# Kernel tuning notes

Measured on AMD Instinct MI355X. Metric: run time of the kernel, lower is better.

## Reference

```python
import jax, jax.numpy as jnp
import numpy as np

B, C, N, M = 4, 256, 4096, 4096
H, D = 4, 64  # num_heads, head_dim = C // H


def _proj(x, W, b):
    # Conv1d(kernel_size=1): pointwise linear over channel dim. x:(B,Cin,L) W:(Cout,Cin) b:(Cout,)
    return jnp.einsum('oc,bcn->bon', W, x) + b[None, :, None]


def setup_inputs() -> dict:
    key = jax.random.key(0)
    ks = jax.random.split(key, 10)
    s = 1.0 / np.sqrt(C)
    return {
        'query': jax.random.normal(ks[0], (B, C, N), dtype=jnp.float32),
        'source': jax.random.normal(ks[1], (B, C, M), dtype=jnp.float32),
        'Wq': jax.random.normal(ks[2], (C, C), dtype=jnp.float32) * s,
        'bq': jnp.zeros((C,), dtype=jnp.float32),
        'Wk': jax.random.normal(ks[3], (C, C), dtype=jnp.float32) * s,
        'bk': jnp.zeros((C,), dtype=jnp.float32),
        'Wv': jax.random.normal(ks[4], (C, C), dtype=jnp.float32) * s,
        'bv': jnp.zeros((C,), dtype=jnp.float32),
        'Wm': jax.random.normal(ks[5], (C, C), dtype=jnp.float32) * s,
        'bm': jnp.zeros((C,), dtype=jnp.float32),
    }


def reference(query, source, Wq, bq, Wk, bk, Wv, bv, Wm, bm):
    b = query.shape[0]
    n = query.shape[-1]
    Q = _proj(query, Wq, bq).reshape(b, H, D, -1)   # (B,H,D,N)
    K = _proj(source, Wk, bk).reshape(b, H, D, -1)  # (B,H,D,M)
    V = _proj(source, Wv, bv).reshape(b, H, D, -1)  # (B,H,D,M)
    scores = jnp.einsum('bhdn,bhdm->bhnm', Q, K) / (D ** 0.5)
    attn = jax.nn.softmax(scores, axis=-1)
    out = jnp.einsum('bhnm,bhdm->bhdn', attn, V)    # (B,H,D,N)
    out = out.reshape(b, H * D, n)                   # (B,C,N)
    return _proj(out, Wm, bm)
```

## Files before the change

### kernel.cpp

```cpp
#include <hip/hip_runtime.h>
#include <hip/hip_bf16.h>
#include <stdint.h>

#define BB 4
#define CCH 256
#define NN 4096
#define MM 4096
#define HH 4
#define DDIM 64

typedef __attribute__((ext_vector_type(8))) short short8v;
typedef __attribute__((ext_vector_type(4))) float f32x4;
typedef __attribute__((ext_vector_type(16))) float f32x16;

__device__ __forceinline__ unsigned short f2b(float f) {
    unsigned int u = __builtin_bit_cast(unsigned int, f);
    unsigned int r = (u + 0x7FFFu + ((u >> 16) & 1u)) >> 16;
    return (unsigned short)r;
}

__device__ __forceinline__ f32x16 zero16() {
    f32x16 z;
#pragma unroll
    for (int i = 0; i < 16; i++) z[i] = 0.f;
    return z;
}

__global__ __launch_bounds__(256) void convert_kernel(
    const float* __restrict__ q, const float* __restrict__ s,
    const float* __restrict__ Wq, const float* __restrict__ Wk,
    const float* __restrict__ Wv, const float* __restrict__ Wm,
    unsigned short* __restrict__ XTq, unsigned short* __restrict__ XTs,
    unsigned short* __restrict__ Wb) {
    __shared__ float tile[64][65];
    const int bid = blockIdx.x, tid = threadIdx.x;
    if (bid < 2048) {
        const float* in = (bid < 1024) ? q : s;
        unsigned short* out = (bid < 1024) ? XTq : XTs;
        const int r = bid & 1023;
        const int b = r >> 8;
        const int rr = r & 255;
        const int l0 = (rr >> 2) * 64, c0 = (rr & 3) * 64;
#pragma unroll
        for (int i = 0; i < 16; i++) {
            int idx = tid + (i << 8);
            int cc = idx >> 6, ll = idx & 63;
            tile[cc][ll] = in[(size_t)(b * CCH + c0 + cc) * 4096 + l0 + ll];
        }
        __syncthreads();
#pragma unroll
        for (int i = 0; i < 16; i++) {
            int idx = tid + (i << 8);
            int ll = idx >> 6, cc = idx & 63;
            out[((size_t)(b * 4096 + l0 + ll) << 8) + c0 + cc] = f2b(tile[cc][ll]);
        }
    } else {
        const int wid = bid - 2048;
        const int wsel = wid >> 4;
        const float* src = (wsel == 0) ? Wq : (wsel == 1) ? Wk : (wsel == 2) ? Wv : Wm;
        const int off = (wid & 15) * 4096;
#pragma unroll
        for (int i = 0; i < 16; i++) {
            int idx = off + tid + (i << 8);
            Wb[(size_t)wsel * 65536 + idx] = f2b(src[idx]);
        }
    }
}

template <int OUTMODE, bool AHEAD>
__device__ __forceinline__ void gemm_body(const unsigned short* __restrict__ XT,
                                          const unsigned short* __restrict__ W,
                                          const float* __restrict__ bias,
                                          void* __restrict__ outv) {
    constexpr int WSTR = 264;
    constexpr int XSTR = 40;
    __shared__ __align__(16) unsigned short Wlds[64 * WSTR];
    __shared__ __align__(16) unsigned short Xlds[256 * XSTR];
    const int tid = threadIdx.x, w = tid >> 6, l = tid & 63;
    const int lg = l >> 4, lm = l & 15;
    const int n0 = blockIdx.x * 256, o0 = blockIdx.y * 64;
    const int oh = (w >> 1) * 32, nh = (w & 1) * 128;

#pragma unroll
    for (int i = 0; i < 8; i++) {
        int idx = tid + (i << 8);
        int row = idx >> 5, c8 = (idx & 31) * 8;
        *(uint4*)&Wlds[row * WSTR + c8] = *(const uint4*)&W[(size_t)(o0 + row) * 256 + c8];
    }

    f32x4 acc[8][2];
#pragma unroll
    for (int nt = 0; nt < 8; nt++)
#pragma unroll
        for (int ot = 0; ot < 2; ot++) acc[nt][ot] = (f32x4){0.f, 0.f, 0.f, 0.f};

    for (int kc = 0; kc < 8; kc++) {
#pragma unroll
        for (int i = 0; i < 4; i++) {
            int idx = tid + (i << 8);
            int row = idx >> 2;
            const unsigned short* srcp;
            if constexpr (AHEAD) {
                int c = kc * 32 + (idx & 3) * 8;
                srcp = XT + ((size_t)(c >> 6) * 4096 + n0 + row) * 64 + (c & 63);
            } else {
                srcp = XT + (size_t)(n0 + row) * 256 + kc * 32 + (idx & 3) * 8;
            }
            *(uint4*)&Xlds[row * XSTR + (idx & 3) * 8] = *(const uint4*)srcp;
        }
        __syncthreads();
        short8v bfrag[2];
#pragma unroll
        for (int ot = 0; ot < 2; ot++)
            bfrag[ot] = *(const short8v*)&Wlds[(oh + ot * 16 + lm) * WSTR + kc * 32 + lg * 8];
#pragma unroll
        for (int nt = 0; nt < 8; nt++) {
            short8v af = *(const short8v*)&Xlds[(nh + nt * 16 + lm) * XSTR + lg * 8];
            acc[nt][0] = __builtin_amdgcn_mfma_f32_16x16x32_bf16(af, bfrag[0], acc[nt][0], 0, 0, 0);
            acc[nt][1] = __builtin_amdgcn_mfma_f32_16x16x32_bf16(af, bfrag[1], acc[nt][1], 0, 0, 0);
        }
        __syncthreads();
    }

#pragma unroll
    for (int nt = 0; nt < 8; nt++)
#pragma unroll
        for (int ot = 0; ot < 2; ot++) {
            int o = o0 + oh + ot * 16 + lm;
            int nb = n0 + nh + nt * 16 + lg * 4;
            float bb = bias[o];
            if constexpr (OUTMODE == 2) {
                float* out = (float*)outv;
                float4 v = make_float4(acc[nt][ot][0] + bb, acc[nt][ot][1] + bb,
                                       acc[nt][ot][2] + bb, acc[nt][ot][3] + bb);
                *(float4*)&out[(size_t)o * 4096 + nb] = v;
            } else if constexpr (OUTMODE == 0) {
                unsigned short* out = (unsigned short*)outv;
                __align__(8) unsigned short v[4];
#pragma unroll
                for (int t = 0; t < 4; t++) v[t] = f2b(acc[nt][ot][t] + bb);
                *(uint2*)&out[(size_t)o * 4096 + nb] = *(uint2*)v;
            } else {
                unsigned short* out = (unsigned short*)outv;
                unsigned short* outp = out + ((size_t)(o >> 6) * 4096 + nb) * 64 + (o & 63);
#pragma unroll
                for (int t = 0; t < 4; t++) outp[t * 64] = f2b(acc[nt][ot][t] + bb);
            }
        }
}

__global__ __launch_bounds__(256) void gemm_qkv_kernel(
    const unsigned short* __restrict__ XTq, const unsigned short* __restrict__ XTs,
    const unsigned short* __restrict__ Wb,
    const float* __restrict__ bq, const float* __restrict__ bk, const float* __restrict__ bv,
    unsigned short* __restrict__ QT, unsigned short* __restrict__ KT,
    unsigned short* __restrict__ Vn) {
    const int z = blockIdx.z;
    const int b = z / 3, p = z - b * 3;
    const unsigned short* XT = ((p == 0) ? XTq : XTs) + (size_t)b * 4096 * 256;
    const unsigned short* W = Wb + p * 65536;
    const float* bias = (p == 0) ? bq : (p == 1) ? bk : bv;
    if (p == 2) {
        gemm_body<0, false>(XT, W, bias, Vn + (size_t)b * 256 * 4096);
    } else {
        unsigned short* out = ((p == 0) ? QT : KT) + (size_t)b * 1048576;
        gemm_body<1, false>(XT, W, bias, out);
    }
}

__global__ __launch_bounds__(256) void gemm_final_kernel(
    const unsigned short* __restrict__ OH, const unsigned short* __restrict__ Wm,
    const float* __restrict__ bm, float* __restrict__ out) {
    const int b = blockIdx.z;
    gemm_body<2, true>(OH + (size_t)b * 1048576, Wm, bm, out + (size_t)b * 256 * 4096);
}

__device__ __forceinline__ void stage_kv(const unsigned short* __restrict__ Kb,
                                         const unsigned short* __restrict__ Vb,
                                         char* dst, int m0s, int tid) {
    char* dK = dst;
    char* dV = dst + 8192;
#pragma unroll
    for (int i = 0; i < 2; i++) {
        int ch = tid + (i << 8);
        int rr = ch >> 3, pp = ch & 7;
        int sw = (pp ^ (rr & 7)) << 4;
        const char* sK = (const char*)(Kb + ((size_t)(m0s + rr) << 6)) + sw;
        const char* sV = (const char*)(Vb + (size_t)rr * 4096 + m0s) + sw;
        __builtin_amdgcn_global_load_lds(
            (const __attribute__((address_space(1))) unsigned int*)sK,
            (__attribute__((address_space(3))) unsigned int*)(dK + (ch << 4)), 16, 0, 0);
        __builtin_amdgcn_global_load_lds(
            (const __attribute__((address_space(1))) unsigned int*)sV,
            (__attribute__((address_space(3))) unsigned int*)(dV + (ch << 4)), 16, 0, 0);
    }
}

__global__ __launch_bounds__(256, 1) void attn_kernel(
    const unsigned short* __restrict__ QT, const unsigned short* __restrict__ KT,
    const unsigned short* __restrict__ Vn, unsigned short* __restrict__ OH) {
    __shared__ __align__(16) char smem[32768];
    const int tid = threadIdx.x, w = tid >> 6, l = tid & 63;
    const int lo5 = l & 31, hi = l >> 5;
    const int bh = blockIdx.y, b = bh >> 2, h = bh & 3;
    const int q0 = blockIdx.x * 256 + w * 64;
    const float s2 = 0.125f * 1.44269504f;

    short8v qf[2][4];
#pragma unroll
    for (int nc = 0; nc < 2; nc++) {
        size_t qrow = ((size_t)bh * 4096 + q0 + nc * 32 + lo5) * 64;
#pragma unroll
        for (int c = 0; c < 4; c++)
            qf[nc][c] = *(const short8v*)&QT[qrow + c * 16 + hi * 8];
    }

    const unsigned short* Vb = Vn + ((size_t)b * 256 + h * 64) * 4096;
    const unsigned short* Kb = KT + (size_t)bh * 262144;

    f32x16 o[2][2];
#pragma unroll
    for (int dc = 0; dc < 2; dc++)
#pragma unroll
        for (int nc = 0; nc < 2; nc++) o[dc][nc] = zero16();
    float mrun[2] = {-1e30f, -1e30f}, lrun[2] = {0.f, 0.f};

    stage_kv(Kb, Vb, smem, 0, tid);

    for (int it = 0; it < 64; it++) {
        __syncthreads();
        char* cur = smem + ((it & 1) << 14);
        if (it < 63) stage_kv(Kb, Vb, smem + (((it + 1) & 1) << 14), (it + 1) * 64, tid);

        short8v kf[2][4];
#pragma unroll
        for (int mc = 0; mc < 2; mc++) {
            int m = mc * 32 + lo5;
#pragma unroll
            for (int c = 0; c < 4; c++)
                kf[mc][c] = *(const short8v*)(cur + m * 128 + (((c * 2 + hi) * 16) ^ ((m & 7) << 4)));
        }
        short8v vf[2][4];
#pragma unroll
        for (int dc = 0; dc < 2; dc++) {
            int d = dc * 32 + lo5;
#pragma unroll
            for (int c = 0; c < 4; c++)
                vf[dc][c] = *(const short8v*)(cur + 8192 + d * 128 + (((c * 2 + hi) * 16) ^ ((d & 7) << 4)));
        }

        f32x16 s[2][2];
#pragma unroll
        for (int nc = 0; nc < 2; nc++)
#pragma unroll
            for (int mc = 0; mc < 2; mc++) {
                f32x16 a = zero16();
#pragma unroll
                for (int c = 0; c < 4; c++)
                    a = __builtin_amdgcn_mfma_f32_32x32x16_bf16(kf[mc][c], qf[nc][c], a, 0, 0, 0);
                s[nc][mc] = a;
            }

        float mxs[2];
#pragma unroll
        for (int nc = 0; nc < 2; nc++) {
            float tv[16];
#pragma unroll
            for (int r = 0; r < 16; r++) tv[r] = fmaxf(s[nc][0][r], s[nc][1][r]);
#pragma unroll
            for (int st = 8; st > 0; st >>= 1)
#pragma unroll
                for (int r = 0; r < st; r++) tv[r] = fmaxf(tv[r], tv[r + st]);
            float mx = fmaxf(tv[0], __shfl_xor(tv[0], 32));
            mxs[nc] = mx * s2;
        }
        if (__any((mxs[0] > mrun[0] + 8.f) || (mxs[1] > mrun[1] + 8.f))) {
#pragma unroll
            for (int nc = 0; nc < 2; nc++) {
                float mn = fmaxf(mrun[nc], mxs[nc]);
                float al = exp2f(mrun[nc] - mn);
                mrun[nc] = mn;
                lrun[nc] *= al;
#pragma unroll
                for (int dc = 0; dc < 2; dc++) o[dc][nc] = o[dc][nc] * al;
            }
        }

#pragma unroll
        for (int nc = 0; nc < 2; nc++) {
            float ls0 = 0.f, ls1 = 0.f, ls2 = 0.f, ls3 = 0.f;
            unsigned int pw[2][8];
#pragma unroll
            for (int mc = 0; mc < 2; mc++) {
                float p[16];
#pragma unroll
                for (int r = 0; r < 16; r++)
                    p[r] = exp2f(fmaf(s[nc][mc][r], s2, -mrun[nc]));
#pragma unroll
                for (int r = 0; r < 4; r++) {
                    ls0 += p[r];
                    ls1 += p[r + 4];
                    ls2 += p[r + 8];
                    ls3 += p[r + 12];
                }
#pragma unroll
                for (int half = 0; half < 2; half++)
#pragma unroll
                    for (int wdx = 0; wdx < 2; wdx++) {
                        unsigned int a, bq;
                        asm("v_cvt_pk_bf16_f32 %0, %1, %2"
                            : "=v"(a) : "v"(p[half * 8 + 2 * wdx]), "v"(p[half * 8 + 2 * wdx + 1]));
                        asm("v_cvt_pk_bf16_f32 %0, %1, %2"
                            : "=v"(bq) : "v"(p[half * 8 + 4 + 2 * wdx]), "v"(p[half * 8 + 4 + 2 * wdx + 1]));
                        asm volatile("v_permlane32_swap_b32 %0, %1" : "+v"(a), "+v"(bq));
                        pw[mc][half * 4 + wdx] = a;
                        pw[mc][half * 4 + wdx + 2] = bq;
                    }
            }
            lrun[nc] += (ls0 + ls1) + (ls2 + ls3);
#pragma unroll
            for (int dc = 0; dc < 2; dc++)
#pragma unroll
                for (int mc = 0; mc < 2; mc++)
#pragma unroll
                    for (int half = 0; half < 2; half++) {
                        union { unsigned int u[4]; short8v v; } pu;
#pragma unroll
                        for (int t = 0; t < 4; t++) pu.u[t] = pw[mc][half * 4 + t];
                        o[dc][nc] = __builtin_amdgcn_mfma_f32_32x32x16_bf16(
                            vf[dc][2 * mc + half], pu.v, o[dc][nc], 0, 0, 0);
                    }
        }
    }

    float inv[2];
#pragma unroll
    for (int nc = 0; nc < 2; nc++) {
        float lt = lrun[nc] + __shfl_xor(lrun[nc], 32);
        inv[nc] = 1.f / lt;
    }
    __syncthreads();
#pragma unroll
    for (int nc = 0; nc < 2; nc++) {
        int row = w * 64 + nc * 32 + lo5;
        char* rbase = smem + row * 128;
        int sw = (row & 7) << 4;
#pragma unroll
        for (int dc = 0; dc < 2; dc++)
#pragma unroll
            for (int g = 0; g < 4; g++) {
                ushort4 v4;
                v4.x = f2b(o[dc][nc][g * 4 + 0] * inv[nc]);
                v4.y = f2b(o[dc][nc][g * 4 + 1] * inv[nc]);
                v4.z = f2b(o[dc][nc][g * 4 + 2] * inv[nc]);
                v4.w = f2b(o[dc][nc][g * 4 + 3] * inv[nc]);
                int colb = dc * 64 + g * 16 + hi * 8;
                *(ushort4*)(rbase + (colb ^ sw)) = v4;
            }
    }
    __syncthreads();
    {
        int row = tid;
        size_t gbase = ((size_t)bh * 4096 + blockIdx.x * 256 + row) * 64;
        int sw = (row & 7) << 4;
#pragma unroll
        for (int ch = 0; ch < 8; ch++) {
            uint4 v = *(const uint4*)(smem + row * 128 + ((ch * 16) ^ sw));
            *(uint4*)&OH[gbase + ch * 8] = v;
        }
    }
}

extern "C" void kernel_launch(void* const* d_in, const int* in_sizes, int n_in,
                              void* d_out, int out_size, void* d_ws, size_t ws_size,
                              hipStream_t stream) {
    const float* q  = (const float*)d_in[0];
    const float* s  = (const float*)d_in[1];
    const float* Wq = (const float*)d_in[2];
    const float* bq = (const float*)d_in[3];
    const float* Wk = (const float*)d_in[4];
    const float* bk = (const float*)d_in[5];
    const float* Wv = (const float*)d_in[6];
    const float* bv = (const float*)d_in[7];
    const float* Wm = (const float*)d_in[8];
    const float* bm = (const float*)d_in[9];
    float* out = (float*)d_out;
    char* ws = (char*)d_ws;

    const size_t SZ = (size_t)BB * 4096 * 256 * 2;
    unsigned short* XTq  = (unsigned short*)(ws);
    unsigned short* XTs  = (unsigned short*)(ws + SZ);
    unsigned short* Wb   = (unsigned short*)(ws + 2 * SZ);
    unsigned short* QT   = (unsigned short*)(ws + 2 * SZ + 524288);
    unsigned short* KTh  = (unsigned short*)(ws + 3 * SZ + 524288);
    unsigned short* Vnat = (unsigned short*)(ws + 4 * SZ + 524288);
    unsigned short* OH   = XTq;

    convert_kernel<<<2112, 256, 0, stream>>>(q, s, Wq, Wk, Wv, Wm, XTq, XTs, Wb);
    gemm_qkv_kernel<<<dim3(16, 4, 12), 256, 0, stream>>>(XTq, XTs, Wb, bq, bk, bv,
                                                         QT, KTh, Vnat);
    attn_kernel<<<dim3(16, 16), 256, 0, stream>>>(QT, KTh, Vnat, OH);
    gemm_final_kernel<<<dim3(16, 4, 4), 256, 0, stream>>>(OH, Wb + 3 * 65536, bm, out);
}
```

Baseline: 273.7 us.

## Use 512-thread attention blocks with one query tile per wave; fold softmax scale into Q

```diff
diff --git a/kernel.cpp b/kernel.cpp
--- a/kernel.cpp
+++ b/kernel.cpp
@@ -71,7 +71,7 @@
 __device__ __forceinline__ void gemm_body(const unsigned short* __restrict__ XT,
                                           const unsigned short* __restrict__ W,
                                           const float* __restrict__ bias,
-                                          void* __restrict__ outv) {
+                                          void* __restrict__ outv, float oscale) {
     constexpr int WSTR = 264;
     constexpr int XSTR = 40;
     __shared__ __align__(16) unsigned short Wlds[64 * WSTR];
@@ -144,7 +144,7 @@
                 unsigned short* out = (unsigned short*)outv;
                 unsigned short* outp = out + ((size_t)(o >> 6) * 4096 + nb) * 64 + (o & 63);
 #pragma unroll
-                for (int t = 0; t < 4; t++) outp[t * 64] = f2b(acc[nt][ot][t] + bb);
+                for (int t = 0; t < 4; t++) outp[t * 64] = f2b((acc[nt][ot][t] + bb) * oscale);
             }
         }
 }
@@ -161,10 +161,10 @@
     const unsigned short* W = Wb + p * 65536;
     const float* bias = (p == 0) ? bq : (p == 1) ? bk : bv;
     if (p == 2) {
-        gemm_body<0, false>(XT, W, bias, Vn + (size_t)b * 256 * 4096);
+        gemm_body<0, false>(XT, W, bias, Vn + (size_t)b * 256 * 4096, 1.0f);
     } else {
         unsigned short* out = ((p == 0) ? QT : KT) + (size_t)b * 1048576;
-        gemm_body<1, false>(XT, W, bias, out);
+        gemm_body<1, false>(XT, W, bias, out, (p == 0) ? 0.1803368801f : 1.0f);
     }
 }
 
@@ -172,58 +172,48 @@
     const unsigned short* __restrict__ OH, const unsigned short* __restrict__ Wm,
     const float* __restrict__ bm, float* __restrict__ out) {
     const int b = blockIdx.z;
-    gemm_body<2, true>(OH + (size_t)b * 1048576, Wm, bm, out + (size_t)b * 256 * 4096);
+    gemm_body<2, true>(OH + (size_t)b * 1048576, Wm, bm, out + (size_t)b * 256 * 4096, 1.0f);
 }
 
 __device__ __forceinline__ void stage_kv(const unsigned short* __restrict__ Kb,
                                          const unsigned short* __restrict__ Vb,
                                          char* dst, int m0s, int tid) {
-    char* dK = dst;
-    char* dV = dst + 8192;
-#pragma unroll
-    for (int i = 0; i < 2; i++) {
-        int ch = tid + (i << 8);
-        int rr = ch >> 3, pp = ch & 7;
-        int sw = (pp ^ (rr & 7)) << 4;
-        const char* sK = (const char*)(Kb + ((size_t)(m0s + rr) << 6)) + sw;
-        const char* sV = (const char*)(Vb + (size_t)rr * 4096 + m0s) + sw;
-        __builtin_amdgcn_global_load_lds(
-            (const __attribute__((address_space(1))) unsigned int*)sK,
-            (__attribute__((address_space(3))) unsigned int*)(dK + (ch << 4)), 16, 0, 0);
-        __builtin_amdgcn_global_load_lds(
-            (const __attribute__((address_space(1))) unsigned int*)sV,
-            (__attribute__((address_space(3))) unsigned int*)(dV + (ch << 4)), 16, 0, 0);
-    }
-}
-
-__global__ __launch_bounds__(256, 1) void attn_kernel(
+    const int rr = tid >> 3, pp = tid & 7;
+    const int sw = (pp ^ (rr & 7)) << 4;
+    const char* sK = (const char*)(Kb + ((size_t)(m0s + rr) << 6)) + sw;
+    const char* sV = (const char*)(Vb + (size_t)rr * 4096 + m0s) + sw;
+    __builtin_amdgcn_global_load_lds(
+        (const __attribute__((address_space(1))) unsigned int*)sK,
+        (__attribute__((address_space(3))) unsigned int*)(dst + (tid << 4)), 16, 0, 0);
+    __builtin_amdgcn_global_load_lds(
+        (const __attribute__((address_space(1))) unsigned int*)sV,
+        (__attribute__((address_space(3))) unsigned int*)(dst + 8192 + (tid << 4)), 16, 0, 0);
+}
+
+__global__ __launch_bounds__(512, 2) void attn_kernel(
     const unsigned short* __restrict__ QT, const unsigned short* __restrict__ KT,
     const unsigned short* __restrict__ Vn, unsigned short* __restrict__ OH) {
     __shared__ __align__(16) char smem[32768];
     const int tid = threadIdx.x, w = tid >> 6, l = tid & 63;
     const int lo5 = l & 31, hi = l >> 5;
     const int bh = blockIdx.y, b = bh >> 2, h = bh & 3;
-    const int q0 = blockIdx.x * 256 + w * 64;
-    const float s2 = 0.125f * 1.44269504f;
-
-    short8v qf[2][4];
-#pragma unroll
-    for (int nc = 0; nc < 2; nc++) {
-        size_t qrow = ((size_t)bh * 4096 + q0 + nc * 32 + lo5) * 64;
+    const int q0 = blockIdx.x * 256 + w * 32;
+
+    short8v qf[4];
+    {
+        size_t qrow = ((size_t)bh * 4096 + q0 + lo5) * 64;
 #pragma unroll
         for (int c = 0; c < 4; c++)
-            qf[nc][c] = *(const short8v*)&QT[qrow + c * 16 + hi * 8];
+            qf[c] = *(const short8v*)&QT[qrow + c * 16 + hi * 8];
     }
 
     const unsigned short* Vb = Vn + ((size_t)b * 256 + h * 64) * 4096;
     const unsigned short* Kb = KT + (size_t)bh * 262144;
 
-    f32x16 o[2][2];
-#pragma unroll
-    for (int dc = 0; dc < 2; dc++)
-#pragma unroll
-        for (int nc = 0; nc < 2; nc++) o[dc][nc] = zero16();
-    float mrun[2] = {-1e30f, -1e30f}, lrun[2] = {0.f, 0.f};
+    f32x16 o[2];
+    o[0] = zero16();
+    o[1] = zero16();
+    float mrun = -1e30f, lrun = 0.f;
 
     stage_kv(Kb, Vb, smem, 0, tid);
 
@@ -249,100 +239,82 @@
                 vf[dc][c] = *(const short8v*)(cur + 8192 + d * 128 + (((c * 2 + hi) * 16) ^ ((d & 7) << 4)));
         }
 
-        f32x16 s[2][2];
-#pragma unroll
-        for (int nc = 0; nc < 2; nc++)
-#pragma unroll
-            for (int mc = 0; mc < 2; mc++) {
-                f32x16 a = zero16();
-#pragma unroll
-                for (int c = 0; c < 4; c++)
-                    a = __builtin_amdgcn_mfma_f32_32x32x16_bf16(kf[mc][c], qf[nc][c], a, 0, 0, 0);
-                s[nc][mc] = a;
+        f32x16 s[2];
+#pragma unroll
+        for (int mc = 0; mc < 2; mc++) {
+            f32x16 a = zero16();
+#pragma unroll
+            for (int c = 0; c < 4; c++)
+                a = __builtin_amdgcn_mfma_f32_32x32x16_bf16(kf[mc][c], qf[c], a, 0, 0, 0);
+            s[mc] = a;
+        }
+
+        float tv[16];
+#pragma unroll
+        for (int r = 0; r < 16; r++) tv[r] = fmaxf(s[0][r], s[1][r]);
+#pragma unroll
+        for (int st = 8; st > 0; st >>= 1)
+#pragma unroll
+            for (int r = 0; r < st; r++) tv[r] = fmaxf(tv[r], tv[r + st]);
+        float mx = fmaxf(tv[0], __shfl_xor(tv[0], 32));
+
+        if (__any(mx > mrun + 8.f)) {
+            float mn = fmaxf(mrun, mx);
+            float al = exp2f(mrun - mn);
+            mrun = mn;
+            lrun *= al;
+            o[0] = o[0] * al;
+            o[1] = o[1] * al;
+        }
+
+        float ls0 = 0.f, ls1 = 0.f, ls2 = 0.f, ls3 = 0.f;
+        unsigned int pw[2][8];
+#pragma unroll
+        for (int mc = 0; mc < 2; mc++) {
+            float p[16];
+#pragma unroll
+            for (int r = 0; r < 16; r++) p[r] = exp2f(s[mc][r] - mrun);
+#pragma unroll
+            for (int r = 0; r < 4; r++) {
+                ls0 += p[r];
+                ls1 += p[r + 4];
+                ls2 += p[r + 8];
+                ls3 += p[r + 12];
             }
-
-        float mxs[2];
-#pragma unroll
-        for (int nc = 0; nc < 2; nc++) {
-            float tv[16];
-#pragma unroll
-            for (int r = 0; r < 16; r++) tv[r] = fmaxf(s[nc][0][r], s[nc][1][r]);
-#pragma unroll
-            for (int st = 8; st > 0; st >>= 1)
-#pragma unroll
-                for (int r = 0; r < st; r++) tv[r] = fmaxf(tv[r], tv[r + st]);
-            float mx = fmaxf(tv[0], __shfl_xor(tv[0], 32));
-            mxs[nc] = mx * s2;
-        }
-        if (__any((mxs[0] > mrun[0] + 8.f) || (mxs[1] > mrun[1] + 8.f))) {
-#pragma unroll
-            for (int nc = 0; nc < 2; nc++) {
-                float mn = fmaxf(mrun[nc], mxs[nc]);
-                float al = exp2f(mrun[nc] - mn);
-                mrun[nc] = mn;
-                lrun[nc] *= al;
-#pragma unroll
-                for (int dc = 0; dc < 2; dc++) o[dc][nc] = o[dc][nc] * al;
-            }
-        }
-
-#pragma unroll
-        for (int nc = 0; nc < 2; nc++) {
-            float ls0 = 0.f, ls1 = 0.f, ls2 = 0.f, ls3 = 0.f;
-            unsigned int pw[2][8];
-#pragma unroll
-            for (int mc = 0; mc < 2; mc++) {
-                float p[16];
-#pragma unroll
-                for (int r = 0; r < 16; r++)
-                    p[r] = exp2f(fmaf(s[nc][mc][r], s2, -mrun[nc]));
-#pragma unroll
-                for (int r = 0; r < 4; r++) {
-                    ls0 += p[r];
-                    ls1 += p[r + 4];
-                    ls2 += p[r + 8];
-                    ls3 += p[r + 12];
+#pragma unroll
+            for (int half = 0; half < 2; half++)
+#pragma unroll
+                for (int wdx = 0; wdx < 2; wdx++) {
+                    unsigned int a, bq;
+                    asm("v_cvt_pk_bf16_f32 %0, %1, %2"
+                        : "=v"(a) : "v"(p[half * 8 + 2 * wdx]), "v"(p[half * 8 + 2 * wdx + 1]));
+                    asm("v_cvt_pk_bf16_f32 %0, %1, %2"
+                        : "=v"(bq) : "v"(p[half * 8 + 4 + 2 * wdx]), "v"(p[half * 8 + 4 + 2 * wdx + 1]));
+                    asm volatile("v_permlane32_swap_b32 %0, %1" : "+v"(a), "+v"(bq));
+                    pw[mc][half * 4 + wdx] = a;
+                    pw[mc][half * 4 + wdx + 2] = bq;
                 }
-#pragma unroll
-                for (int half = 0; half < 2; half++)
-#pragma unroll
-                    for (int wdx = 0; wdx < 2; wdx++) {
-                        unsigned int a, bq;
-                        asm("v_cvt_pk_bf16_f32 %0, %1, %2"
-                            : "=v"(a) : "v"(p[half * 8 + 2 * wdx]), "v"(p[half * 8 + 2 * wdx + 1]));
-                        asm("v_cvt_pk_bf16_f32 %0, %1, %2"
-                            : "=v"(bq) : "v"(p[half * 8 + 4 + 2 * wdx]), "v"(p[half * 8 + 4 + 2 * wdx + 1]));
-                        asm volatile("v_permlane32_swap_b32 %0, %1" : "+v"(a), "+v"(bq));
-                        pw[mc][half * 4 + wdx] = a;
-                        pw[mc][half * 4 + wdx + 2] = bq;
-                    }
-            }
-            lrun[nc] += (ls0 + ls1) + (ls2 + ls3);
-#pragma unroll
-            for (int dc = 0; dc < 2; dc++)
-#pragma unroll
-                for (int mc = 0; mc < 2; mc++)
-#pragma unroll
-                    for (int half = 0; half < 2; half++) {
-                        union { unsigned int u[4]; short8v v; } pu;
-#pragma unroll
-                        for (int t = 0; t < 4; t++) pu.u[t] = pw[mc][half * 4 + t];
-                        o[dc][nc] = __builtin_amdgcn_mfma_f32_32x32x16_bf16(
-                            vf[dc][2 * mc + half], pu.v, o[dc][nc], 0, 0, 0);
-                    }
-        }
-    }
-
-    float inv[2];
-#pragma unroll
-    for (int nc = 0; nc < 2; nc++) {
-        float lt = lrun[nc] + __shfl_xor(lrun[nc], 32);
-        inv[nc] = 1.f / lt;
-    }
+        }
+        lrun += (ls0 + ls1) + (ls2 + ls3);
+#pragma unroll
+        for (int dc = 0; dc < 2; dc++)
+#pragma unroll
+            for (int mc = 0; mc < 2; mc++)
+#pragma unroll
+                for (int half = 0; half < 2; half++) {
+                    union { unsigned int u[4]; short8v v; } pu;
+#pragma unroll
+                    for (int t = 0; t < 4; t++) pu.u[t] = pw[mc][half * 4 + t];
+                    o[dc] = __builtin_amdgcn_mfma_f32_32x32x16_bf16(
+                        vf[dc][2 * mc + half], pu.v, o[dc], 0, 0, 0);
+                }
+    }
+
+    float lt = lrun + __shfl_xor(lrun, 32);
+    float inv = 1.f / lt;
     __syncthreads();
-#pragma unroll
-    for (int nc = 0; nc < 2; nc++) {
-        int row = w * 64 + nc * 32 + lo5;
+    {
+        int row = w * 32 + lo5;
         char* rbase = smem + row * 128;
         int sw = (row & 7) << 4;
 #pragma unroll
@@ -350,22 +322,22 @@
 #pragma unroll
             for (int g = 0; g < 4; g++) {
                 ushort4 v4;
-                v4.x = f2b(o[dc][nc][g * 4 + 0] * inv[nc]);
-                v4.y = f2b(o[dc][nc][g * 4 + 1] * inv[nc]);
-                v4.z = f2b(o[dc][nc][g * 4 + 2] * inv[nc]);
-                v4.w = f2b(o[dc][nc][g * 4 + 3] * inv[nc]);
+                v4.x = f2b(o[dc][g * 4 + 0] * inv);
+                v4.y = f2b(o[dc][g * 4 + 1] * inv);
+                v4.z = f2b(o[dc][g * 4 + 2] * inv);
+                v4.w = f2b(o[dc][g * 4 + 3] * inv);
                 int colb = dc * 64 + g * 16 + hi * 8;
                 *(ushort4*)(rbase + (colb ^ sw)) = v4;
             }
     }
     __syncthreads();
     {
-        int row = tid;
-        size_t gbase = ((size_t)bh * 4096 + blockIdx.x * 256 + row) * 64;
+        int row = tid >> 1, seg = (tid & 1) * 64;
+        size_t gbase = ((size_t)bh * 4096 + blockIdx.x * 256 + row) * 64 + (size_t)(tid & 1) * 32;
         int sw = (row & 7) << 4;
 #pragma unroll
-        for (int ch = 0; ch < 8; ch++) {
-            uint4 v = *(const uint4*)(smem + row * 128 + ((ch * 16) ^ sw));
+        for (int ch = 0; ch < 4; ch++) {
+            uint4 v = *(const uint4*)(smem + row * 128 + ((seg + ch * 16) ^ sw));
             *(uint4*)&OH[gbase + ch * 8] = v;
         }
     }
@@ -399,6 +371,6 @@
     convert_kernel<<<2112, 256, 0, stream>>>(q, s, Wq, Wk, Wv, Wm, XTq, XTs, Wb);
     gemm_qkv_kernel<<<dim3(16, 4, 12), 256, 0, stream>>>(XTq, XTs, Wb, bq, bk, bv,
                                                          QT, KTh, Vnat);
-    attn_kernel<<<dim3(16, 16), 256, 0, stream>>>(QT, KTh, Vnat, OH);
+    attn_kernel<<<dim3(16, 16), 512, 0, stream>>>(QT, KTh, Vnat, OH);
     gemm_final_kernel<<<dim3(16, 4, 4), 256, 0, stream>>>(OH, Wb + 3 * 65536, bm, out);
 }
```

After: 249.1 us. -9.0%, faster.
